# Kernel optimization log

Measured on AMD Instinct MI355X. Metric: run time of the kernel, lower is better.

Reference implementation:

```python
import jax, jax.numpy as jnp
import numpy as np

B, T, N, H = 4, 256, 16, 256
NHEAD = 8
FFN = 1024
WIN = 8
EPS = 1e-5


def setup_inputs() -> dict:
    key = jax.random.key(0)
    ks = jax.random.split(key, 10)
    s = 0.02
    return {
        "x": jax.random.normal(ks[0], (B, T, N, H), dtype=jnp.float32),
        "key_padding_mask": jnp.zeros((B, T, N), dtype=bool),
        "Wq": jax.random.normal(ks[1], (H, H), dtype=jnp.float32) * s,
        "bq": jnp.zeros((H,), dtype=jnp.float32),
        "Wk": jax.random.normal(ks[2], (H, H), dtype=jnp.float32) * s,
        "bk": jnp.zeros((H,), dtype=jnp.float32),
        "Wv": jax.random.normal(ks[3], (H, H), dtype=jnp.float32) * s,
        "bv": jnp.zeros((H,), dtype=jnp.float32),
        "W1": jax.random.normal(ks[4], (H, FFN), dtype=jnp.float32) * s,
        "b1": jnp.zeros((FFN,), dtype=jnp.float32),
        "W2": jax.random.normal(ks[5], (FFN, H), dtype=jnp.float32) * s,
        "b2": jnp.zeros((H,), dtype=jnp.float32),
        "g1": jnp.ones((H,), dtype=jnp.float32),
        "beta1": jnp.zeros((H,), dtype=jnp.float32),
        "g2": jnp.ones((H,), dtype=jnp.float32),
        "beta2": jnp.zeros((H,), dtype=jnp.float32),
    }


def _layer_norm(x, g, b):
    m = jnp.mean(x, axis=-1, keepdims=True)
    v = jnp.mean(jnp.square(x - m), axis=-1, keepdims=True)
    return (x - m) * jax.lax.rsqrt(v + EPS) * g + b


def reference(x, key_padding_mask, Wq, bq, Wk, bk, Wv, bv, W1, b1, W2, b2, g1, beta1, g2, beta2):
    Bq, Tq, Nq, Hq = x.shape
    D = Hq // NHEAD
    W = 2 * WIN + 1
    # projections
    q = (x @ Wq + bq).reshape(Bq, Tq, Nq, NHEAD, D) / np.float32(np.sqrt(D))
    k = (x @ Wk + bk).reshape(Bq, Tq, Nq, NHEAD, D)
    v = (x @ Wv + bv).reshape(Bq, Tq, Nq, NHEAD, D)
    idx = jnp.arange(Tq)[:, None] + jnp.arange(W)[None, :] - WIN  # (T, W)
    valid = (idx >= 0) & (idx < Tq)                               # (T, W)
    cidx = jnp.clip(idx, 0, Tq - 1)
    vf6 = valid.reshape(1, Tq, W, 1, 1, 1).astype(q.dtype)
    # gathered window keys/values, zero outside clip: (B, T, W, N, h, D)
    wk = jnp.take(k, cidx, axis=1) * vf6
    wv = jnp.take(v, cidx, axis=1) * vf6
    # attention logits over (W, N) neighbors per head
    logits = jnp.einsum('btnhd,btwmhd->btnwmh', q, wk)  # (B,T,N,W,N,h)
    # mask: padded detections within window, plus out-of-range frames
    kpm_g = jnp.take(key_padding_mask, cidx, axis=1)          # (B,T,W,N)
    mask = jnp.where(valid[None, :, :, None], kpm_g, True)    # (B,T,W,N)
    logits = jnp.where(mask[:, :, None, :, :, None], -jnp.inf, logits)
    attn = jax.nn.softmax(logits.reshape(Bq, Tq, Nq, W * Nq, NHEAD), axis=-2)
    ctx = jnp.einsum('btnmh,btmhd->btnhd', attn,
                     wv.reshape(Bq, Tq, W * Nq, NHEAD, D)).reshape(Bq, Tq, Nq, Hq)
    # residual + LN + FFN + residual + LN (dropout = identity in eval)
    y = _layer_norm(x + ctx, g1, beta1)
    ff = jax.nn.relu(y @ W1 + b1) @ W2 + b2
    return _layer_norm(y + ff, g2, beta2)
```

## Files before the change

kernel.cpp:

```cpp
#include <hip/hip_runtime.h>
#include <hip/hip_bf16.h>
#include <math.h>

typedef __attribute__((ext_vector_type(8))) short short8;
typedef __attribute__((ext_vector_type(4))) float float4v;

#define BB 4
#define TT 256
#define NDET 16
#define HH 256
#define NHEAD 8
#define DD 32
#define FFNDIM 1024
#define ROWS (BB*TT*NDET)
#define EPS 1e-5f

__device__ __forceinline__ unsigned short f2bf(float f) {
  unsigned int u = __float_as_uint(f);
  u += 0x7fffu + ((u >> 16) & 1u);
  return (unsigned short)(u >> 16);
}
__device__ __forceinline__ float bf2f(unsigned short u) {
  return __uint_as_float((unsigned int)u << 16);
}
__device__ __forceinline__ float exp2v(float x) {
  float r; asm("v_exp_f32 %0, %1" : "=v"(r) : "v"(x)); return r;
}
__device__ __forceinline__ unsigned int cvtpk(float lo, float hi) {
  unsigned int r; asm("v_cvt_pk_bf16_f32 %0, %1, %2" : "=v"(r) : "v"(lo), "v"(hi)); return r;
}

__device__ __forceinline__ void wt_tile(const float* __restrict__ W, unsigned short* __restrict__ WT,
                                        int K, int N, int k0, int n0,
                                        float (*tile)[33], int tid) {
  {
    int r = tid >> 3, c4 = (tid & 7) * 4;
    float4 in = *(const float4*)(W + (size_t)(k0 + r) * N + n0 + c4);
    tile[r][c4 + 0] = in.x; tile[r][c4 + 1] = in.y;
    tile[r][c4 + 2] = in.z; tile[r][c4 + 3] = in.w;
  }
  __syncthreads();
  {
    int n = tid >> 3, k4 = (tid & 7) * 4;
    ushort4 o;
    o.x = f2bf(tile[k4 + 0][n]); o.y = f2bf(tile[k4 + 1][n]);
    o.z = f2bf(tile[k4 + 2][n]); o.w = f2bf(tile[k4 + 3][n]);
    *(ushort4*)(WT + (size_t)(n0 + n) * K + k0 + k4) = o;
  }
}

__global__ void prep_kernel(const float* __restrict__ x, const unsigned char* __restrict__ kpm,
                            const float* __restrict__ Wq, const float* __restrict__ Wk,
                            const float* __restrict__ Wv, const float* __restrict__ W1,
                            const float* __restrict__ W2,
                            const float* __restrict__ bq, const float* __restrict__ bk,
                            const float* __restrict__ bv,
                            unsigned short* __restrict__ xb, unsigned short* __restrict__ WqkvT,
                            unsigned short* __restrict__ W1T, unsigned short* __restrict__ W2T,
                            unsigned short* __restrict__ kpm16, float* __restrict__ bqkv) {
  __shared__ float tile[32][33];
  int bid = blockIdx.x, tid = threadIdx.x;
  if (bid < 4096) {
    size_t i = (size_t)(bid * 256 + tid) * 4;
    float4 v = *(const float4*)(x + i);
    ushort4 o = { f2bf(v.x), f2bf(v.y), f2bf(v.z), f2bf(v.w) };
    *(ushort4*)(xb + i) = o;
  } else if (bid < 4288) {
    int t = bid - 4096;
    int wsel = t >> 6, tt = t & 63;
    const float* W = (wsel == 0) ? Wq : (wsel == 1) ? Wk : Wv;
    wt_tile(W, WqkvT + wsel * 65536, 256, 256, (tt >> 3) * 32, (tt & 7) * 32, tile, tid);
  } else if (bid < 4544) {
    int tt = bid - 4288;
    wt_tile(W1, W1T, 256, 1024, (tt >> 5) * 32, (tt & 31) * 32, tile, tid);
  } else if (bid < 4800) {
    int tt = bid - 4544;
    wt_tile(W2, W2T, 1024, 256, (tt >> 3) * 32, (tt & 7) * 32, tile, tid);
  } else if (bid < 4804) {
    int w = (bid - 4800) * 256 + tid;
    uint4 u = *(const uint4*)(kpm + (size_t)w * 16);
    unsigned int a[4] = {u.x, u.y, u.z, u.w};
    unsigned int bits = 0;
#pragma unroll
    for (int m = 0; m < 16; ++m)
      if ((a[m >> 2] >> ((m & 3) * 8)) & 0xffu) bits |= (1u << m);
    kpm16[w] = (unsigned short)bits;
  } else {
    bqkv[tid] = bq[tid];
    bqkv[256 + tid] = bk[tid];
    bqkv[512 + tid] = bv[tid];
  }
}

template<int NROWS, int K, int NT>
__device__ __forceinline__ void stage_rows(const unsigned short* __restrict__ src, int kcol0,
                                           char* ldsbase, int tid) {
  constexpr int ISS = NROWS * 8 / NT;
  int wave = tid >> 6;
#pragma unroll
  for (int i = 0; i < ISS; ++i) {
    int flat = i * (NT * 16) + tid * 16;
    int r = flat >> 7;
    int cb = flat & 127;
    int scb = cb ^ ((r & 7) << 4);
    const unsigned short* g = src + (size_t)r * K + kcol0 + (scb >> 1);
    char* l = ldsbase + i * (NT * 16) + wave * 1024;
    __builtin_amdgcn_global_load_lds((const __attribute__((address_space(1))) void*)g,
                                     (__attribute__((address_space(3))) void*)l, 16, 0, 0);
  }
}

template<int EPI>
__launch_bounds__(256, 2)
__global__ void gemm_kernel(const unsigned short* __restrict__ A,
                            const unsigned short* __restrict__ Bt,
                            const float* __restrict__ bias,
                            unsigned short* __restrict__ q_o, unsigned short* __restrict__ k_o,
                            unsigned short* __restrict__ vT_o,
                            unsigned short* __restrict__ outb) {
  constexpr int BM = 128, BN = 128, K = 256, KP = K / 64;
  __shared__ char smem[(BM + BN) * 128];
  const int tid = threadIdx.x;
  const int wave = tid >> 6, lane = tid & 63;
  const int lrow = lane & 15, g = lane >> 4;
  const int m0 = blockIdx.x * BM;
  const int n0 = blockIdx.y * BN;
  const int wr = wave >> 1, wc = wave & 1;
  char* As = smem;
  char* Bs = smem + BM * 128;
  float4v acc[4][4];
#pragma unroll
  for (int i = 0; i < 4; ++i)
#pragma unroll
    for (int j = 0; j < 4; ++j) acc[i][j] = (float4v){0.f, 0.f, 0.f, 0.f};

  const unsigned short* Abase = A + (size_t)m0 * K;
  const unsigned short* Bbase = Bt + (size_t)n0 * K;
  for (int ph = 0; ph < KP; ++ph) {
    if (ph) __syncthreads();
    stage_rows<BM, K, 256>(Abase, ph * 64, As, tid);
    stage_rows<BN, K, 256>(Bbase, ph * 64, Bs, tid);
    __syncthreads();
#pragma unroll
    for (int ks = 0; ks < 2; ++ks) {
      short8 af[4], bf[4];
#pragma unroll
      for (int i = 0; i < 4; ++i) {
        int ar = wr * 64 + i * 16 + lrow;
        af[i] = *(const short8*)(As + ar * 128 + ((ks * 64 + g * 16) ^ ((ar & 7) << 4)));
      }
#pragma unroll
      for (int j = 0; j < 4; ++j) {
        int br = wc * 64 + j * 16 + lrow;
        bf[j] = *(const short8*)(Bs + br * 128 + ((ks * 64 + g * 16) ^ ((br & 7) << 4)));
      }
#pragma unroll
      for (int i = 0; i < 4; ++i)
#pragma unroll
        for (int j = 0; j < 4; ++j)
          acc[i][j] = __builtin_amdgcn_mfma_f32_16x16x32_bf16(af[i], bf[j], acc[i][j], 0, 0, 0);
    }
  }

  if (EPI == 0) {
    const float QS = 0.17677669529663687f * 1.4426950408889634f;
#pragma unroll
    for (int i = 0; i < 4; ++i)
#pragma unroll
      for (int j = 0; j < 4; ++j) {
        int C = n0 + wc * 64 + j * 16 + lrow;
        float bv = bias[C];
        int proj = C >> 8, cc = C & 255;
        int h = cc >> 5, d = cc & 31;
        if (proj == 2) {
          int grow0 = m0 + wr * 64 + i * 16 + g * 4;
          int b = grow0 >> 12, tn0 = grow0 & 4095;
          ushort4 o;
          o.x = f2bf(acc[i][j][0] + bv);
          o.y = f2bf(acc[i][j][1] + bv);
          o.z = f2bf(acc[i][j][2] + bv);
          o.w = f2bf(acc[i][j][3] + bv);
          *(ushort4*)(vT_o + ((size_t)(b * 8 + h) * 32 + d) * 4096 + tn0) = o;
        } else {
          unsigned short* om = (proj == 0) ? q_o : k_o;
          float sc = (proj == 0) ? QS : 1.f;
#pragma unroll
          for (int r = 0; r < 4; ++r) {
            int grow = m0 + wr * 64 + i * 16 + g * 4 + r;
            int b = grow >> 12, tn = grow & 4095;
            om[(size_t)((b * 8 + h) * 4096 + tn) * 32 + d] = f2bf((acc[i][j][r] + bv) * sc);
          }
        }
      }
  } else {
#pragma unroll
    for (int i = 0; i < 4; ++i)
#pragma unroll
      for (int j = 0; j < 4; ++j) {
        int C = n0 + wc * 64 + j * 16 + lrow;
        float bv = bias[C];
#pragma unroll
        for (int r = 0; r < 4; ++r) {
          int grow = m0 + wr * 64 + i * 16 + g * 4 + r;
          outb[(size_t)grow * FFNDIM + C] = f2bf(fmaxf(acc[i][j][r] + bv, 0.f));
        }
      }
  }
}

__launch_bounds__(512, 4)
__global__ void attn_ln_kernel(const unsigned short* __restrict__ qb,
                               const unsigned short* __restrict__ kb,
                               const unsigned short* __restrict__ vT,
                               const unsigned short* __restrict__ kpm16,
                               const unsigned short* __restrict__ xb,
                               const float* __restrict__ gw, const float* __restrict__ bw,
                               unsigned short* __restrict__ yb) {
  __shared__ char Pall[8][9216];
  __shared__ float stats[8][16][2];
  __shared__ float mst[16], rst[16];
  int tid = threadIdx.x;
  int wave = tid >> 6, l = tid & 63;
  int t = blockIdx.x & 255, b = blockIdx.x >> 8;
  char* P = Pall[wave];
  int lrow = l & 15, g = l >> 4;
  int swz = (lrow & 3) << 4;
  size_t base = (size_t)(b * 8 + wave) * 4096;
  short8 qf = *(const short8*)(qb + (base + t * 16 + lrow) * 32 + g * 8);
  const float4v z4 = {0.f, 0.f, 0.f, 0.f};
  float4v s[17];
  float mx = -INFINITY;
#pragma unroll
  for (int w = 0; w < 17; ++w) {
    int j = t + w - 8;
    if (j >= 0 && j < 256) {
      short8 kf = *(const short8*)(kb + (base + j * 16 + lrow) * 32 + g * 8);
      float4v sv = __builtin_amdgcn_mfma_f32_16x16x32_bf16(kf, qf, z4, 0, 0, 0);
      unsigned int mw = kpm16[b * 256 + j];
#pragma unroll
      for (int r = 0; r < 4; ++r)
        if ((mw >> (g * 4 + r)) & 1u) sv[r] = -INFINITY;
      s[w] = sv;
#pragma unroll
      for (int r = 0; r < 4; ++r) mx = fmaxf(mx, sv[r]);
    } else {
      s[w] = (float4v){-INFINITY, -INFINITY, -INFINITY, -INFINITY};
    }
  }
  mx = fmaxf(mx, __shfl_xor(mx, 16));
  mx = fmaxf(mx, __shfl_xor(mx, 32));
  float sum = 0.f;
#pragma unroll
  for (int w = 0; w < 17; ++w)
#pragma unroll
    for (int r = 0; r < 4; ++r) {
      float e = exp2v(s[w][r] - mx);
      s[w][r] = e; sum += e;
    }
  sum += __shfl_xor(sum, 16);
  sum += __shfl_xor(sum, 32);
  float inv = 1.f / sum;
#pragma unroll
  for (int w = 0; w < 17; ++w) {
    unsigned int u0 = cvtpk(s[w][0], s[w][1]);
    unsigned int u1 = cvtpk(s[w][2], s[w][3]);
    *(unsigned int*)(P + lrow * 576 + (((w * 16 + g * 4 + 0) * 2) ^ swz)) = u0;
    *(unsigned int*)(P + lrow * 576 + (((w * 16 + g * 4 + 2) * 2) ^ swz)) = u1;
  }
  *(unsigned int*)(P + lrow * 576 + (((272 + g * 4 + 0) * 2) ^ swz)) = 0u;
  *(unsigned int*)(P + lrow * 576 + (((272 + g * 4 + 2) * 2) ^ swz)) = 0u;

  size_t rowbase = (size_t)(b * 256 + t) * 16 * 256;
  int col = wave * 32 + lrow;
  float xv0[4], xv1[4];
#pragma unroll
  for (int r = 0; r < 4; ++r) {
    xv0[r] = bf2f(xb[rowbase + (g * 4 + r) * 256 + col]);
    xv1[r] = bf2f(xb[rowbase + (g * 4 + r) * 256 + col + 16]);
  }

  asm volatile("s_waitcnt lgkmcnt(0)" ::: "memory");
  __builtin_amdgcn_sched_barrier(0);
  float4v o0 = z4, o1 = z4;
  int tn0 = (t - 8) * 16;
  const unsigned short* vbase = vT + (base * 32 / 4096 + lrow) * 4096;
  __builtin_amdgcn_s_setprio(1);
#pragma unroll
  for (int c = 0; c < 9; ++c) {
    short8 pf = *(const short8*)(P + lrow * 576 + ((c * 64 + g * 16) ^ swz));
    short8 v0 = *(const short8*)(vbase + tn0 + c * 32 + g * 8);
    short8 v1 = *(const short8*)(vbase + (size_t)16 * 4096 + tn0 + c * 32 + g * 8);
    o0 = __builtin_amdgcn_mfma_f32_16x16x32_bf16(pf, v0, o0, 0, 0, 0);
    o1 = __builtin_amdgcn_mfma_f32_16x16x32_bf16(pf, v1, o1, 0, 0, 0);
  }
  __builtin_amdgcn_s_setprio(0);

  float va0[4], va1[4];
#pragma unroll
  for (int r = 0; r < 4; ++r) {
    float invn = __shfl(inv, g * 4 + r);
    va0[r] = o0[r] * invn + xv0[r];
    va1[r] = o1[r] * invn + xv1[r];
  }
#pragma unroll
  for (int r = 0; r < 4; ++r) {
    float sm = va0[r] + va1[r];
    float sq = va0[r] * va0[r] + va1[r] * va1[r];
#pragma unroll
    for (int off = 1; off < 16; off <<= 1) {
      sm += __shfl_xor(sm, off);
      sq += __shfl_xor(sq, off);
    }
    if (lrow == 0) {
      stats[wave][g * 4 + r][0] = sm;
      stats[wave][g * 4 + r][1] = sq;
    }
  }
  __syncthreads();
  if (tid < 16) {
    float S = 0.f, Q = 0.f;
#pragma unroll
    for (int w2 = 0; w2 < 8; ++w2) { S += stats[w2][tid][0]; Q += stats[w2][tid][1]; }
    float mean = S * (1.f / 256.f);
    float var = Q * (1.f / 256.f) - mean * mean;
    mst[tid] = mean;
    rst[tid] = rsqrtf(var + EPS);
  }
  __syncthreads();
  float gv0 = gw[col], gv1 = gw[col + 16];
  float bv0 = bw[col], bv1 = bw[col + 16];
#pragma unroll
  for (int r = 0; r < 4; ++r) {
    int row = g * 4 + r;
    float mean = mst[row], rs = rst[row];
    yb[rowbase + row * 256 + col]      = f2bf((va0[r] - mean) * rs * gv0 + bv0);
    yb[rowbase + row * 256 + col + 16] = f2bf((va1[r] - mean) * rs * gv1 + bv1);
  }
}

__launch_bounds__(512, 2)
__global__ void ffn2_kernel(const unsigned short* __restrict__ hid,
                            const unsigned short* __restrict__ W2T,
                            const float* __restrict__ b2,
                            const unsigned short* __restrict__ yb,
                            const float* __restrict__ gw, const float* __restrict__ bw,
                            float* __restrict__ out) {
  constexpr int BM = 64, BN = 256, K = 1024, KP = K / 64;
  __shared__ char smem[(BM + BN) * 128];
  __shared__ float stats[8][32][2];
  __shared__ float mst[64], rst[64];
  const int tid = threadIdx.x;
  const int wave = tid >> 6, lane = tid & 63;
  const int lrow = lane & 15, g = lane >> 4;
  const int m0 = blockIdx.x * BM;
  const int wr = wave >> 2, wc = wave & 3;
  char* As = smem;
  char* Bs = smem + BM * 128;
  float4v acc[2][4];
#pragma unroll
  for (int i = 0; i < 2; ++i)
#pragma unroll
    for (int j = 0; j < 4; ++j) acc[i][j] = (float4v){0.f, 0.f, 0.f, 0.f};

  const unsigned short* Abase = hid + (size_t)m0 * K;
  for (int ph = 0; ph < KP; ++ph) {
    if (ph) __syncthreads();
    stage_rows<BM, K, 512>(Abase, ph * 64, As, tid);
    stage_rows<BN, K, 512>(W2T, ph * 64, Bs, tid);
    __syncthreads();
#pragma unroll
    for (int ks = 0; ks < 2; ++ks) {
      short8 af[2], bf[4];
#pragma unroll
      for (int i = 0; i < 2; ++i) {
        int ar = wr * 32 + i * 16 + lrow;
        af[i] = *(const short8*)(As + ar * 128 + ((ks * 64 + g * 16) ^ ((ar & 7) << 4)));
      }
#pragma unroll
      for (int j = 0; j < 4; ++j) {
        int br = wc * 64 + j * 16 + lrow;
        bf[j] = *(const short8*)(Bs + br * 128 + ((ks * 64 + g * 16) ^ ((br & 7) << 4)));
      }
#pragma unroll
      for (int i = 0; i < 2; ++i)
#pragma unroll
        for (int j = 0; j < 4; ++j)
          acc[i][j] = __builtin_amdgcn_mfma_f32_16x16x32_bf16(af[i], bf[j], acc[i][j], 0, 0, 0);
    }
  }
  __syncthreads();

#pragma unroll
  for (int i = 0; i < 2; ++i)
#pragma unroll
    for (int j = 0; j < 4; ++j) {
      int col = wc * 64 + j * 16 + lrow;
      float bv = b2[col];
#pragma unroll
      for (int r = 0; r < 4; ++r) {
        int row = wr * 32 + i * 16 + g * 4 + r;
        acc[i][j][r] += bv + bf2f(yb[(size_t)(m0 + row) * 256 + col]);
      }
    }
#pragma unroll
  for (int i = 0; i < 2; ++i)
#pragma unroll
    for (int r = 0; r < 4; ++r) {
      float sm = acc[i][0][r] + acc[i][1][r] + acc[i][2][r] + acc[i][3][r];
      float sq = acc[i][0][r] * acc[i][0][r] + acc[i][1][r] * acc[i][1][r]
               + acc[i][2][r] * acc[i][2][r] + acc[i][3][r] * acc[i][3][r];
#pragma unroll
      for (int off = 1; off < 16; off <<= 1) {
        sm += __shfl_xor(sm, off);
        sq += __shfl_xor(sq, off);
      }
      if (lrow == 0) {
        stats[wave][i * 16 + g * 4 + r][0] = sm;
        stats[wave][i * 16 + g * 4 + r][1] = sq;
      }
    }
  __syncthreads();
  if (tid < 64) {
    int wrr = tid >> 5, rl = tid & 31;
    float S = 0.f, Q = 0.f;
#pragma unroll
    for (int w2 = 0; w2 < 4; ++w2) {
      S += stats[wrr * 4 + w2][rl][0];
      Q += stats[wrr * 4 + w2][rl][1];
    }
    float mean = S * (1.f / 256.f);
    float var = Q * (1.f / 256.f) - mean * mean;
    mst[tid] = mean;
    rst[tid] = rsqrtf(var + EPS);
  }
  __syncthreads();
  float gv[4], bev[4];
#pragma unroll
  for (int j = 0; j < 4; ++j) {
    int col = wc * 64 + j * 16 + lrow;
    gv[j] = gw[col]; bev[j] = bw[col];
  }
#pragma unroll
  for (int i = 0; i < 2; ++i)
#pragma unroll
    for (int r = 0; r < 4; ++r) {
      int rl = wr * 32 + i * 16 + g * 4 + r;
      float mean = mst[rl], rs = rst[rl];
#pragma unroll
      for (int j = 0; j < 4; ++j) {
        int col = wc * 64 + j * 16 + lrow;
        out[(size_t)(m0 + rl) * 256 + col] = (acc[i][j][r] - mean) * rs * gv[j] + bev[j];
      }
    }
}

extern "C" void kernel_launch(void* const* d_in, const int* in_sizes, int n_in,
                              void* d_out, int out_size, void* d_ws, size_t ws_size,
                              hipStream_t stream) {
  const float* x  = (const float*)d_in[0];
  const unsigned char* kpm = (const unsigned char*)d_in[1];
  const float* Wq = (const float*)d_in[2];
  const float* bq = (const float*)d_in[3];
  const float* Wk = (const float*)d_in[4];
  const float* bk = (const float*)d_in[5];
  const float* Wv = (const float*)d_in[6];
  const float* bv = (const float*)d_in[7];
  const float* W1 = (const float*)d_in[8];
  const float* b1 = (const float*)d_in[9];
  const float* W2 = (const float*)d_in[10];
  const float* b2 = (const float*)d_in[11];
  const float* g1 = (const float*)d_in[12];
  const float* be1= (const float*)d_in[13];
  const float* g2 = (const float*)d_in[14];
  const float* be2= (const float*)d_in[15];
  float* out = (float*)d_out;

  char* w = (char*)d_ws;
  const size_t MB = 1u << 20;
  unsigned short* xb   = (unsigned short*)(w);
  unsigned short* qhm  = (unsigned short*)(w + 8 * MB);
  unsigned short* khm  = (unsigned short*)(w + 16 * MB);
  unsigned short* vTb  = (unsigned short*)(w + 24 * MB);
  unsigned short* yb   = (unsigned short*)(w + 48 * MB);
  unsigned short* WqkvT = (unsigned short*)(w + 72 * MB);
  unsigned short* W1T = WqkvT + 196608;
  unsigned short* W2T = W1T + 262144;
  unsigned short* kpm16 = W2T + 262144;
  float* bqkv = (float*)(kpm16 + 1024);
  unsigned short* hid = qhm;

  prep_kernel<<<4805, 256, 0, stream>>>(x, kpm, Wq, Wk, Wv, W1, W2, bq, bk, bv,
                                        xb, WqkvT, W1T, W2T, kpm16, bqkv);
  gemm_kernel<0><<<dim3(128, 6), 256, 0, stream>>>(xb, WqkvT, bqkv, qhm, khm, vTb, nullptr);
  attn_ln_kernel<<<1024, 512, 0, stream>>>(qhm, khm, vTb, kpm16, xb, g1, be1, yb);
  gemm_kernel<1><<<dim3(128, 8), 256, 0, stream>>>(yb, W1T, b1, nullptr, nullptr, nullptr, hid);
  ffn2_kernel<<<256, 512, 0, stream>>>(hid, W2T, b2, yb, g2, be2, out);
}
```

Baseline: 106.9 us.

## Feed softmax probabilities directly from registers into 16x16x16 MFMA, drop LDS staging

```diff
diff --git a/kernel.cpp b/kernel.cpp
--- a/kernel.cpp
+++ b/kernel.cpp
@@ -3,6 +3,7 @@
 #include <math.h>
 
 typedef __attribute__((ext_vector_type(8))) short short8;
+typedef __attribute__((ext_vector_type(4))) short short4v;
 typedef __attribute__((ext_vector_type(4))) float float4v;
 
 #define BB 4
@@ -28,6 +29,18 @@
 }
 __device__ __forceinline__ unsigned int cvtpk(float lo, float hi) {
   unsigned int r; asm("v_cvt_pk_bf16_f32 %0, %1, %2" : "=v"(r) : "v"(lo), "v"(hi)); return r;
+}
+__device__ __forceinline__ float4v mfma16(short4v a, short4v b, float4v c) {
+#if __has_builtin(__builtin_amdgcn_mfma_f32_16x16x16bf16_1k)
+  return __builtin_amdgcn_mfma_f32_16x16x16bf16_1k(a, b, c, 0, 0, 0);
+#elif __has_builtin(__builtin_amdgcn_mfma_f32_16x16x16_bf16)
+  return __builtin_amdgcn_mfma_f32_16x16x16_bf16(a, b, c, 0, 0, 0);
+#else
+  float4v d;
+  asm("v_mfma_f32_16x16x16_bf16 %0, %1, %2, %3"
+      : "=v"(d) : "v"(a), "v"(b), "v"(c));
+  return d;
+#endif
 }
 
 __device__ __forceinline__ void wt_tile(const float* __restrict__ W, unsigned short* __restrict__ WT,
@@ -216,15 +229,13 @@
                                const unsigned short* __restrict__ xb,
                                const float* __restrict__ gw, const float* __restrict__ bw,
                                unsigned short* __restrict__ yb) {
-  __shared__ char Pall[8][9216];
   __shared__ float stats[8][16][2];
   __shared__ float mst[16], rst[16];
   int tid = threadIdx.x;
   int wave = tid >> 6, l = tid & 63;
-  int t = blockIdx.x & 255, b = blockIdx.x >> 8;
-  char* P = Pall[wave];
+  int lid = (blockIdx.x & 7) * 128 + (blockIdx.x >> 3);
+  int t = lid & 255, b = lid >> 8;
   int lrow = l & 15, g = l >> 4;
-  int swz = (lrow & 3) << 4;
   size_t base = (size_t)(b * 8 + wave) * 4096;
   short8 qf = *(const short8*)(qb + (base + t * 16 + lrow) * 32 + g * 8);
   const float4v z4 = {0.f, 0.f, 0.f, 0.f};
@@ -260,15 +271,6 @@
   sum += __shfl_xor(sum, 16);
   sum += __shfl_xor(sum, 32);
   float inv = 1.f / sum;
-#pragma unroll
-  for (int w = 0; w < 17; ++w) {
-    unsigned int u0 = cvtpk(s[w][0], s[w][1]);
-    unsigned int u1 = cvtpk(s[w][2], s[w][3]);
-    *(unsigned int*)(P + lrow * 576 + (((w * 16 + g * 4 + 0) * 2) ^ swz)) = u0;
-    *(unsigned int*)(P + lrow * 576 + (((w * 16 + g * 4 + 2) * 2) ^ swz)) = u1;
-  }
-  *(unsigned int*)(P + lrow * 576 + (((272 + g * 4 + 0) * 2) ^ swz)) = 0u;
-  *(unsigned int*)(P + lrow * 576 + (((272 + g * 4 + 2) * 2) ^ swz)) = 0u;
 
   size_t rowbase = (size_t)(b * 256 + t) * 16 * 256;
   int col = wave * 32 + lrow;
@@ -279,19 +281,20 @@
     xv1[r] = bf2f(xb[rowbase + (g * 4 + r) * 256 + col + 16]);
   }
 
-  asm volatile("s_waitcnt lgkmcnt(0)" ::: "memory");
-  __builtin_amdgcn_sched_barrier(0);
   float4v o0 = z4, o1 = z4;
   int tn0 = (t - 8) * 16;
-  const unsigned short* vbase = vT + (base * 32 / 4096 + lrow) * 4096;
+  const unsigned short* vb0 = vT + ((size_t)(b * 8 + wave) * 32 + lrow) * 4096 + tn0 + g * 4;
   __builtin_amdgcn_s_setprio(1);
 #pragma unroll
-  for (int c = 0; c < 9; ++c) {
-    short8 pf = *(const short8*)(P + lrow * 576 + ((c * 64 + g * 16) ^ swz));
-    short8 v0 = *(const short8*)(vbase + tn0 + c * 32 + g * 8);
-    short8 v1 = *(const short8*)(vbase + (size_t)16 * 4096 + tn0 + c * 32 + g * 8);
-    o0 = __builtin_amdgcn_mfma_f32_16x16x32_bf16(pf, v0, o0, 0, 0, 0);
-    o1 = __builtin_amdgcn_mfma_f32_16x16x32_bf16(pf, v1, o1, 0, 0, 0);
+  for (int w = 0; w < 17; ++w) {
+    uint2 pu;
+    pu.x = cvtpk(s[w][0], s[w][1]);
+    pu.y = cvtpk(s[w][2], s[w][3]);
+    short4v pw = *(short4v*)&pu;
+    uint2 v0u = *(const uint2*)(vb0 + w * 16);
+    uint2 v1u = *(const uint2*)(vb0 + (size_t)16 * 4096 + w * 16);
+    o0 = mfma16(pw, *(short4v*)&v0u, o0);
+    o1 = mfma16(pw, *(short4v*)&v1u, o1);
   }
   __builtin_amdgcn_s_setprio(0);
 
```

Result: slower. 114.4 us (+7.1%).
